# Optimization experiments

Hardware: AMD Instinct MI355X
Metric: run time of the kernel (lower is better)

Reference implementation:

```python
import jax, jax.numpy as jnp
import numpy as np
import math

B, H, S, D = 2, 16, 2048, 128
COEFF = 2.0  # layer_number


def setup_inputs() -> dict:
    key = jax.random.key(0)
    kq, kk, kv = jax.random.split(key, 3)
    return {
        "query_layer": jax.random.normal(kq, (B, H, S, D), dtype=jnp.float32),
        "key_layer": jax.random.normal(kk, (B, H, S, D), dtype=jnp.float32),
        "value_layer": jax.random.normal(kv, (B, H, S, D), dtype=jnp.float32),
    }


def reference(query_layer, key_layer, value_layer):
    b, h, sq, d = query_layer.shape
    sk = key_layer.shape[2]
    norm_factor = math.sqrt(d) * COEFF
    # raw scores [b,h,sq,sk]; divide by sqrt(d)*coeff, cast fp32, multiply by coeff
    scores = jnp.einsum("bhqd,bhkd->bhqk", query_layer, key_layer) / norm_factor
    scores = scores.astype(jnp.float32) * COEFF
    # causal mask (sq == sk path with attention_mask=None)
    causal = jnp.tril(jnp.ones((sq, sk), dtype=bool))
    scores = jnp.where(causal, scores, jnp.float32(-jnp.inf))
    probs = jax.nn.softmax(scores, axis=-1).astype(value_layer.dtype)
    # dropout p=0.0 -> identity
    ctx = jnp.einsum("bhqk,bhkd->bhqd", probs, value_layer)
    # [b,h,sq,d] -> [b,sq,h*d]
    return ctx.transpose(0, 2, 1, 3).reshape(b, sq, h * d)
```

## Files before the change

### kernel.cpp

```cpp
#include <hip/hip_runtime.h>
#include <hip/hip_bf16.h>
#include <math.h>

#define NB 2
#define NH 16
#define NS 2048
#define ND 128

typedef __bf16 bf16x8 __attribute__((ext_vector_type(8)));
typedef __bf16 bf16x4 __attribute__((ext_vector_type(4)));
typedef float f32x4 __attribute__((ext_vector_type(4)));

__global__ __launch_bounds__(256)
void prep(const float* __restrict__ K, const float* __restrict__ V,
          char* __restrict__ Kb, char* __restrict__ Vb)
{
    if (blockIdx.x < 4096) {
        int g = blockIdx.x * 256 + threadIdx.x;
        const int c8 = g & 15;
        const int row = g >> 4;
        const int s = row & 2047, bh = row >> 11;
        const int jt = s >> 6, r = s & 63;
        const float* src = K + ((size_t)row << 7) + (c8 << 3);
        float4 a = *(const float4*)src;
        float4 c = *(const float4*)(src + 4);
        bf16x8 o;
        o[0]=(__bf16)a.x; o[1]=(__bf16)a.y; o[2]=(__bf16)a.z; o[3]=(__bf16)a.w;
        o[4]=(__bf16)c.x; o[5]=(__bf16)c.y; o[6]=(__bf16)c.z; o[7]=(__bf16)c.w;
        *(bf16x8*)(Kb + (((size_t)(bh*32 + jt)) << 14) + r*256 + ((c8 ^ (r & 7)) << 4)) = o;
    } else {
        const int T    = blockIdx.x - 4096;
        const int w2   = threadIdx.x >> 6;
        const int lane = threadIdx.x & 63;
        const int d0   = lane << 1;
        const float2* vbase = (const float2*)V + ((size_t)T << 12);
        char* ob = Vb + ((size_t)T << 14);
        #pragma unroll
        for (int p = 0; p < 2; ++p) {
            const int kv8 = w2*2 + p;
            bf16x8 o0, o1;
            #pragma unroll
            for (int j = 0; j < 8; ++j) {
                float2 x = vbase[(size_t)(kv8*8 + j)*64 + lane];
                o0[j] = (__bf16)x.x;
                o1[j] = (__bf16)x.y;
            }
            *(bf16x8*)(ob + d0*128       + ((kv8 ^ (d0 & 7)) << 4))       = o0;
            *(bf16x8*)(ob + (d0+1)*128   + ((kv8 ^ ((d0+1) & 7)) << 4))   = o1;
        }
    }
}

__device__ __forceinline__ void gld16(void* lds, const void* gsrc)
{
    __builtin_amdgcn_global_load_lds(
        (const __attribute__((address_space(1))) void*)gsrc,
        (__attribute__((address_space(3))) void*)lds, 16, 0, 0);
}

__global__ __launch_bounds__(256, 2)
void fa_fwd(const float* __restrict__ Qg_, const char* __restrict__ Kb,
            const char* __restrict__ Vb, float* __restrict__ Out)
{
    __shared__ char Kl[2][16384];
    __shared__ char Vl[2][16384];
    __shared__ char Pl[8192];
    __shared__ float Rs[4][64];

    const int tid  = threadIdx.x;
    const int w    = tid >> 6;
    const int lane = tid & 63;
    const int quad = lane >> 4;
    const int l15  = lane & 15;

    const int pr = blockIdx.x >> 5;
    const int bh = blockIdx.x & 31;
    const int b  = bh >> 4, h = bh & 15;
    const int qtA = 31 - pr, qtB = pr;
    const int ntA = qtA + 1;
    const int total = ntA + qtB + 1;
    const int qA = qtA * 64, qB = qtB * 64;

    const float* Qg = Qg_ + (size_t)bh * NS * ND;
    const char*  Kt = Kb + ((size_t)bh << 19);
    const char*  Vt = Vb + ((size_t)bh << 19);

    const int xo = (l15 & 7) << 4;

    const float CSC = 0.08838834764831845f * 1.4426950408889634f;

    bf16x8 qf[4][4];
    auto loadQ = [&](int qbase) {
        #pragma unroll
        for (int nq = 0; nq < 4; ++nq) {
            const float* qp = Qg + (size_t)(qbase + nq*16 + l15) * ND + quad*8;
            #pragma unroll
            for (int ks = 0; ks < 4; ++ks) {
                float4 a = *(const float4*)(qp + ks*32);
                float4 c = *(const float4*)(qp + ks*32 + 4);
                bf16x8 f;
                f[0]=(__bf16)(a.x*CSC); f[1]=(__bf16)(a.y*CSC); f[2]=(__bf16)(a.z*CSC); f[3]=(__bf16)(a.w*CSC);
                f[4]=(__bf16)(c.x*CSC); f[5]=(__bf16)(c.y*CSC); f[6]=(__bf16)(c.z*CSC); f[7]=(__bf16)(c.w*CSC);
                qf[nq][ks] = f;
            }
        }
    };

    f32x4 O[4][2];
    float rs[4];
    #pragma unroll
    for (int m = 0; m < 4; ++m)
        #pragma unroll
        for (int nl = 0; nl < 2; ++nl)
            #pragma unroll
            for (int r = 0; r < 4; ++r) O[m][nl][r] = 0.0f;
    #pragma unroll
    for (int nq = 0; nq < 4; ++nq) rs[nq] = 0.0f;

    auto stage = [&](int jt, int buf) {
        const char* kg = Kt + (((size_t)jt) << 14) + w*4096 + lane*16;
        const char* vg = Vt + (((size_t)jt) << 14) + w*4096 + lane*16;
        char* kl = &Kl[buf][0] + w*4096;
        char* vl = &Vl[buf][0] + w*4096;
        #pragma unroll
        for (int i = 0; i < 4; ++i) {
            gld16(kl + i*1024, kg + i*1024);
            gld16(vl + i*1024, vg + i*1024);
        }
    };

    auto flush = [&](int qb) {
        #pragma unroll
        for (int nq = 0; nq < 4; ++nq) {
            float v = rs[nq];
            v += __shfl_xor(v, 16, 64);
            v += __shfl_xor(v, 32, 64);
            if (quad == 0) Rs[w][nq*16 + l15] = v;
        }
        __syncthreads();
        #pragma unroll
        for (int m = 0; m < 4; ++m) {
            #pragma unroll
            for (int r = 0; r < 4; ++r) {
                int qq = m*16 + quad*4 + r;
                float tt = Rs[0][qq] + Rs[1][qq] + Rs[2][qq] + Rs[3][qq];
                float inv = 1.0f / tt;
                int q = qb + qq;
                float* op = Out + ((size_t)(b*NS + q)) * (NH*ND) + h*ND + l15;
                op[(2*w)*16]   = O[m][0][r] * inv;
                op[(2*w+1)*16] = O[m][1][r] * inv;
            }
        }
    };

    loadQ(qA);
    stage(0, 0);
    int cur = 0;

    for (int t = 0; t < total; ++t) {
        const int phase = (t >= ntA);
        const bool diag = (phase ? (t - ntA) == qtB : t == qtA);

        if (t + 1 < total) {
            const int jt2 = (t + 1 >= ntA) ? (t + 1 - ntA) : (t + 1);
            stage(jt2, cur ^ 1);
            asm volatile("s_waitcnt vmcnt(8)" ::: "memory");
        } else {
            asm volatile("s_waitcnt vmcnt(0)" ::: "memory");
        }
        __builtin_amdgcn_s_barrier();
        asm volatile("" ::: "memory");

        if (t == ntA) {
            flush(qA);
            #pragma unroll
            for (int m = 0; m < 4; ++m)
                #pragma unroll
                for (int nl = 0; nl < 2; ++nl)
                    #pragma unroll
                    for (int r = 0; r < 4; ++r) O[m][nl][r] = 0.0f;
            #pragma unroll
            for (int nq = 0; nq < 4; ++nq) rs[nq] = 0.0f;
            loadQ(qB);
        }

        const char* Kc = &Kl[cur][0] + (w*16 + l15)*256;
        bf16x8 kf[4];
        #pragma unroll
        for (int ks = 0; ks < 4; ++ks)
            kf[ks] = *(const bf16x8*)(Kc + ((((ks*4 + quad) << 4)) ^ xo));
        f32x4 S[4];
        #pragma unroll
        for (int nq = 0; nq < 4; ++nq)
            #pragma unroll
            for (int r = 0; r < 4; ++r) S[nq][r] = 0.0f;
        __builtin_amdgcn_s_setprio(1);
        #pragma unroll
        for (int ks = 0; ks < 4; ++ks)
            #pragma unroll
            for (int nq = 0; nq < 4; ++nq)
                S[nq] = __builtin_amdgcn_mfma_f32_16x16x32_bf16(kf[ks], qf[nq][ks], S[nq], 0, 0, 0);
        __builtin_amdgcn_s_setprio(0);

        const char* Vc = &Vl[cur][0];
        bf16x8 vfr[2][2];
        #pragma unroll
        for (int nl = 0; nl < 2; ++nl)
            #pragma unroll
            for (int ks = 0; ks < 2; ++ks)
                vfr[nl][ks] = *(const bf16x8*)(Vc + ((2*w + nl)*16 + l15)*128 + ((((ks*4 + quad) << 4)) ^ xo));

        #pragma unroll
        for (int nq = 0; nq < 4; ++nq) {
            bf16x4 pk;
            #pragma unroll
            for (int r = 0; r < 4; ++r) {
                float e = exp2f(S[nq][r]);
                if (diag && (w*16 + quad*4 + r > nq*16 + l15)) e = 0.0f;
                rs[nq] += e;
                pk[r] = (__bf16)e;
            }
            *(bf16x4*)(Pl + (nq*16 + l15)*128 + ((((4*w + quad) ^ ((l15 & 7) << 1))) << 3)) = pk;
        }

        asm volatile("s_waitcnt lgkmcnt(0)" ::: "memory");
        __builtin_amdgcn_s_barrier();
        asm volatile("" ::: "memory");

        __builtin_amdgcn_s_setprio(1);
        #pragma unroll
        for (int m = 0; m < 4; ++m) {
            bf16x8 pa0 = *(const bf16x8*)(Pl + (m*16 + l15)*128 + (((quad << 4)) ^ xo));
            bf16x8 pa1 = *(const bf16x8*)(Pl + (m*16 + l15)*128 + ((((4 + quad) << 4)) ^ xo));
            O[m][0] = __builtin_amdgcn_mfma_f32_16x16x32_bf16(pa0, vfr[0][0], O[m][0], 0, 0, 0);
            O[m][1] = __builtin_amdgcn_mfma_f32_16x16x32_bf16(pa0, vfr[1][0], O[m][1], 0, 0, 0);
            O[m][0] = __builtin_amdgcn_mfma_f32_16x16x32_bf16(pa1, vfr[0][1], O[m][0], 0, 0, 0);
            O[m][1] = __builtin_amdgcn_mfma_f32_16x16x32_bf16(pa1, vfr[1][1], O[m][1], 0, 0, 0);
        }
        __builtin_amdgcn_s_setprio(0);

        asm volatile("" ::: "memory");
        __builtin_amdgcn_s_barrier();
        asm volatile("" ::: "memory");
        cur ^= 1;
    }

    flush(qB);
}

extern "C" void kernel_launch(void* const* d_in, const int* in_sizes, int n_in,
                              void* d_out, int out_size, void* d_ws, size_t ws_size,
                              hipStream_t stream) {
    const float* Q = (const float*)d_in[0];
    const float* K = (const float*)d_in[1];
    const float* V = (const float*)d_in[2];
    float* Out = (float*)d_out;
    char* Kb = (char*)d_ws;
    char* Vb = (char*)d_ws + ((size_t)32 << 19);
    prep<<<dim3(5120), dim3(256), 0, stream>>>(K, V, Kb, Vb);
    fa_fwd<<<dim3(512), dim3(256), 0, stream>>>(Q, Kb, Vb, Out);
}
```

Baseline: 202.0 us.

## Rewrite attention kernel with 32x32 MFMA, 128-row Q tiles and register-resident P

Measured after the change: 183.3 us. 1.1x faster.

```diff
diff --git a/kernel.cpp b/kernel.cpp
--- a/kernel.cpp
+++ b/kernel.cpp
@@ -8,8 +8,7 @@
 #define ND 128
 
 typedef __bf16 bf16x8 __attribute__((ext_vector_type(8)));
-typedef __bf16 bf16x4 __attribute__((ext_vector_type(4)));
-typedef float f32x4 __attribute__((ext_vector_type(4)));
+typedef float f32x16 __attribute__((ext_vector_type(16)));
 
 __global__ __launch_bounds__(256)
 void prep(const float* __restrict__ K, const float* __restrict__ V,
@@ -27,12 +26,11 @@
         bf16x8 o;
         o[0]=(__bf16)a.x; o[1]=(__bf16)a.y; o[2]=(__bf16)a.z; o[3]=(__bf16)a.w;
         o[4]=(__bf16)c.x; o[5]=(__bf16)c.y; o[6]=(__bf16)c.z; o[7]=(__bf16)c.w;
-        *(bf16x8*)(Kb + (((size_t)(bh*32 + jt)) << 14) + r*256 + ((c8 ^ (r & 7)) << 4)) = o;
+        *(bf16x8*)(Kb + (((size_t)(bh*32 + jt)) << 14) + r*256 + ((c8 ^ (r & 15)) << 4)) = o;
     } else {
         const int T    = blockIdx.x - 4096;
         const int w2   = threadIdx.x >> 6;
         const int lane = threadIdx.x & 63;
-        const int d0   = lane << 1;
         const float2* vbase = (const float2*)V + ((size_t)T << 12);
         char* ob = Vb + ((size_t)T << 14);
         #pragma unroll
@@ -45,8 +43,8 @@
                 o0[j] = (__bf16)x.x;
                 o1[j] = (__bf16)x.y;
             }
-            *(bf16x8*)(ob + d0*128       + ((kv8 ^ (d0 & 7)) << 4))       = o0;
-            *(bf16x8*)(ob + (d0+1)*128   + ((kv8 ^ ((d0+1) & 7)) << 4))   = o1;
+            *(bf16x8*)(ob + lane*256 + ((kv8 ^ (lane & 15)) << 4))       = o0;
+            *(bf16x8*)(ob + lane*256 + (((8 | kv8) ^ (lane & 15)) << 4)) = o1;
         }
     }
 }
@@ -62,190 +60,166 @@
 void fa_fwd(const float* __restrict__ Qg_, const char* __restrict__ Kb,
             const char* __restrict__ Vb, float* __restrict__ Out)
 {
-    __shared__ char Kl[2][16384];
-    __shared__ char Vl[2][16384];
-    __shared__ char Pl[8192];
-    __shared__ float Rs[4][64];
+    __shared__ char lds_[65536];
 
     const int tid  = threadIdx.x;
     const int w    = tid >> 6;
     const int lane = tid & 63;
-    const int quad = lane >> 4;
-    const int l15  = lane & 15;
-
-    const int pr = blockIdx.x >> 5;
-    const int bh = blockIdx.x & 31;
-    const int b  = bh >> 4, h = bh & 15;
-    const int qtA = 31 - pr, qtB = pr;
-    const int ntA = qtA + 1;
-    const int total = ntA + qtB + 1;
-    const int qA = qtA * 64, qB = qtB * 64;
+    const int l31  = lane & 31;
+    const int h    = lane >> 5;
+
+    const int c  = blockIdx.x;
+    const int bh = c & 31;
+    const int qt = (c < 256) ? (c >> 5) : (23 - (c >> 5));
+    const int b  = bh >> 4, head = bh & 15;
+    const int nt = 2 * (qt + 1);
+    const int qb = qt * 128;
+    const int qw = qb + 32 * w;
 
     const float* Qg = Qg_ + (size_t)bh * NS * ND;
     const char*  Kt = Kb + ((size_t)bh << 19);
     const char*  Vt = Vb + ((size_t)bh << 19);
 
-    const int xo = (l15 & 7) << 4;
+    int kaddr[8], vaddr[4];
+    #pragma unroll
+    for (int ks = 0; ks < 8; ++ks)
+        kaddr[ks] = l31*256 + (((2*ks + h) ^ (lane & 15)) << 4);
+    #pragma unroll
+    for (int ks = 0; ks < 4; ++ks)
+        vaddr[ks] = (l31 >> 1)*256 + (((((lane & 1) << 3) | (2*ks + h)) ^ (l31 >> 1)) << 4);
+
+    auto stage = [&](int t, int buf) {
+        const char* kg = Kt + (((size_t)t) << 14) + tid*16;
+        const char* vg = Vt + (((size_t)t) << 14) + tid*16;
+        char* kl = lds_ + buf*16384 + w*1024;
+        char* vl = lds_ + 32768 + buf*16384 + w*1024;
+        #pragma unroll
+        for (int i = 0; i < 4; ++i) gld16(kl + i*4096, kg + i*4096);
+        #pragma unroll
+        for (int i = 0; i < 4; ++i) gld16(vl + i*4096, vg + i*4096);
+    };
+
+    stage(0, 0);
+    stage(1, 1);
 
     const float CSC = 0.08838834764831845f * 1.4426950408889634f;
-
-    bf16x8 qf[4][4];
-    auto loadQ = [&](int qbase) {
-        #pragma unroll
-        for (int nq = 0; nq < 4; ++nq) {
-            const float* qp = Qg + (size_t)(qbase + nq*16 + l15) * ND + quad*8;
+    bf16x8 qf[8];
+    {
+        const float* qrow = Qg + (size_t)(qb + 32*w + l31) * ND + 8*h;
+        #pragma unroll
+        for (int ks = 0; ks < 8; ++ks) {
+            float4 a = *(const float4*)(qrow + 16*ks);
+            float4 d = *(const float4*)(qrow + 16*ks + 4);
+            bf16x8 f;
+            f[0]=(__bf16)(a.x*CSC); f[1]=(__bf16)(a.y*CSC); f[2]=(__bf16)(a.z*CSC); f[3]=(__bf16)(a.w*CSC);
+            f[4]=(__bf16)(d.x*CSC); f[5]=(__bf16)(d.y*CSC); f[6]=(__bf16)(d.z*CSC); f[7]=(__bf16)(d.w*CSC);
+            qf[ks] = f;
+        }
+    }
+
+    f32x16 O_[4];
+    #pragma unroll
+    for (int db = 0; db < 4; ++db)
+        #pragma unroll
+        for (int r = 0; r < 16; ++r) O_[db][r] = 0.0f;
+    float rs = 0.0f;
+
+    auto compute = [&](int t, int KIMM, int VIMM) {
+        f32x16 S0, S1;
+        #pragma unroll
+        for (int r = 0; r < 16; ++r) { S0[r] = 0.0f; S1[r] = 0.0f; }
+        __builtin_amdgcn_s_setprio(1);
+        #pragma unroll
+        for (int ks = 0; ks < 8; ++ks) {
+            bf16x8 ka = *(const bf16x8*)(lds_ + (kaddr[ks] + KIMM));
+            bf16x8 kb = *(const bf16x8*)(lds_ + (kaddr[ks] + KIMM + 8192));
+            S0 = __builtin_amdgcn_mfma_f32_32x32x16_bf16(ka, qf[ks], S0, 0, 0, 0);
+            S1 = __builtin_amdgcn_mfma_f32_32x32x16_bf16(kb, qf[ks], S1, 0, 0, 0);
+        }
+        __builtin_amdgcn_s_setprio(0);
+
+        if (64*t + 63 > qw) {
+            const int limh = qw + l31 - 64*t - 4*h;
             #pragma unroll
-            for (int ks = 0; ks < 4; ++ks) {
-                float4 a = *(const float4*)(qp + ks*32);
-                float4 c = *(const float4*)(qp + ks*32 + 4);
-                bf16x8 f;
-                f[0]=(__bf16)(a.x*CSC); f[1]=(__bf16)(a.y*CSC); f[2]=(__bf16)(a.z*CSC); f[3]=(__bf16)(a.w*CSC);
-                f[4]=(__bf16)(c.x*CSC); f[5]=(__bf16)(c.y*CSC); f[6]=(__bf16)(c.z*CSC); f[7]=(__bf16)(c.w*CSC);
-                qf[nq][ks] = f;
+            for (int r = 0; r < 16; ++r) {
+                const int k0 = (r & 3) + 8*(r >> 2);
+                if (k0 > limh)      S0[r] = -INFINITY;
+                if (k0 + 32 > limh) S1[r] = -INFINITY;
             }
         }
-    };
-
-    f32x4 O[4][2];
-    float rs[4];
-    #pragma unroll
-    for (int m = 0; m < 4; ++m)
-        #pragma unroll
-        for (int nl = 0; nl < 2; ++nl)
-            #pragma unroll
-            for (int r = 0; r < 4; ++r) O[m][nl][r] = 0.0f;
-    #pragma unroll
-    for (int nq = 0; nq < 4; ++nq) rs[nq] = 0.0f;
-
-    auto stage = [&](int jt, int buf) {
-        const char* kg = Kt + (((size_t)jt) << 14) + w*4096 + lane*16;
-        const char* vg = Vt + (((size_t)jt) << 14) + w*4096 + lane*16;
-        char* kl = &Kl[buf][0] + w*4096;
-        char* vl = &Vl[buf][0] + w*4096;
-        #pragma unroll
-        for (int i = 0; i < 4; ++i) {
-            gld16(kl + i*1024, kg + i*1024);
-            gld16(vl + i*1024, vg + i*1024);
-        }
-    };
-
-    auto flush = [&](int qb) {
-        #pragma unroll
-        for (int nq = 0; nq < 4; ++nq) {
-            float v = rs[nq];
-            v += __shfl_xor(v, 16, 64);
-            v += __shfl_xor(v, 32, 64);
-            if (quad == 0) Rs[w][nq*16 + l15] = v;
-        }
-        __syncthreads();
-        #pragma unroll
-        for (int m = 0; m < 4; ++m) {
-            #pragma unroll
-            for (int r = 0; r < 4; ++r) {
-                int qq = m*16 + quad*4 + r;
-                float tt = Rs[0][qq] + Rs[1][qq] + Rs[2][qq] + Rs[3][qq];
-                float inv = 1.0f / tt;
-                int q = qb + qq;
-                float* op = Out + ((size_t)(b*NS + q)) * (NH*ND) + h*ND + l15;
-                op[(2*w)*16]   = O[m][0][r] * inv;
-                op[(2*w+1)*16] = O[m][1][r] * inv;
-            }
-        }
-    };
-
-    loadQ(qA);
-    stage(0, 0);
-    int cur = 0;
-
-    for (int t = 0; t < total; ++t) {
-        const int phase = (t >= ntA);
-        const bool diag = (phase ? (t - ntA) == qtB : t == qtA);
-
-        if (t + 1 < total) {
-            const int jt2 = (t + 1 >= ntA) ? (t + 1 - ntA) : (t + 1);
-            stage(jt2, cur ^ 1);
-            asm volatile("s_waitcnt vmcnt(8)" ::: "memory");
-        } else {
-            asm volatile("s_waitcnt vmcnt(0)" ::: "memory");
-        }
-        __builtin_amdgcn_s_barrier();
-        asm volatile("" ::: "memory");
-
-        if (t == ntA) {
-            flush(qA);
-            #pragma unroll
-            for (int m = 0; m < 4; ++m)
-                #pragma unroll
-                for (int nl = 0; nl < 2; ++nl)
-                    #pragma unroll
-                    for (int r = 0; r < 4; ++r) O[m][nl][r] = 0.0f;
-            #pragma unroll
-            for (int nq = 0; nq < 4; ++nq) rs[nq] = 0.0f;
-            loadQ(qB);
-        }
-
-        const char* Kc = &Kl[cur][0] + (w*16 + l15)*256;
-        bf16x8 kf[4];
-        #pragma unroll
-        for (int ks = 0; ks < 4; ++ks)
-            kf[ks] = *(const bf16x8*)(Kc + ((((ks*4 + quad) << 4)) ^ xo));
-        f32x4 S[4];
-        #pragma unroll
-        for (int nq = 0; nq < 4; ++nq)
-            #pragma unroll
-            for (int r = 0; r < 4; ++r) S[nq][r] = 0.0f;
+        #pragma unroll
+        for (int r = 0; r < 16; ++r) {
+            float e0 = __builtin_amdgcn_exp2f(S0[r]);
+            float e1 = __builtin_amdgcn_exp2f(S1[r]);
+            rs += e0; rs += e1;
+            S0[r] = e0; S1[r] = e1;
+        }
+        unsigned P0[8], P1[8];
+        #pragma unroll
+        for (int i = 0; i < 8; ++i) {
+            unsigned u0, u1;
+            asm("v_cvt_pk_bf16_f32 %0, %1, %2" : "=v"(u0) : "v"(S0[2*i]), "v"(S0[2*i+1]));
+            asm("v_cvt_pk_bf16_f32 %0, %1, %2" : "=v"(u1) : "v"(S1[2*i]), "v"(S1[2*i+1]));
+            P0[i] = u0; P1[i] = u1;
+        }
+        bf16x8 pa[4];
+        #pragma unroll
+        for (int ks = 0; ks < 4; ++ks) {
+            const int o = 4*(ks & 1);
+            unsigned a0, a1, b0, b1;
+            if (ks < 2) { a0 = P0[o]; a1 = P0[o+1]; b0 = P0[o+2]; b1 = P0[o+3]; }
+            else        { a0 = P1[o]; a1 = P1[o+1]; b0 = P1[o+2]; b1 = P1[o+3]; }
+            asm("v_permlane32_swap_b32 %0, %1" : "+v"(a0), "+v"(b0));
+            asm("v_permlane32_swap_b32 %0, %1" : "+v"(a1), "+v"(b1));
+            union { unsigned u[4]; bf16x8 v; } cv;
+            cv.u[0] = a0; cv.u[1] = a1; cv.u[2] = b0; cv.u[3] = b1;
+            pa[ks] = cv.v;
+        }
         __builtin_amdgcn_s_setprio(1);
         #pragma unroll
         for (int ks = 0; ks < 4; ++ks)
             #pragma unroll
-            for (int nq = 0; nq < 4; ++nq)
-                S[nq] = __builtin_amdgcn_mfma_f32_16x16x32_bf16(kf[ks], qf[nq][ks], S[nq], 0, 0, 0);
+            for (int db = 0; db < 4; ++db) {
+                bf16x8 vf = *(const bf16x8*)(lds_ + (vaddr[ks] + VIMM + db*4096));
+                O_[db] = __builtin_amdgcn_mfma_f32_32x32x16_bf16(pa[ks], vf, O_[db], 0, 0, 0);
+            }
         __builtin_amdgcn_s_setprio(0);
-
-        const char* Vc = &Vl[cur][0];
-        bf16x8 vfr[2][2];
-        #pragma unroll
-        for (int nl = 0; nl < 2; ++nl)
-            #pragma unroll
-            for (int ks = 0; ks < 2; ++ks)
-                vfr[nl][ks] = *(const bf16x8*)(Vc + ((2*w + nl)*16 + l15)*128 + ((((ks*4 + quad) << 4)) ^ xo));
-
-        #pragma unroll
-        for (int nq = 0; nq < 4; ++nq) {
-            bf16x4 pk;
-            #pragma unroll
-            for (int r = 0; r < 4; ++r) {
-                float e = exp2f(S[nq][r]);
-                if (diag && (w*16 + quad*4 + r > nq*16 + l15)) e = 0.0f;
-                rs[nq] += e;
-                pk[r] = (__bf16)e;
-            }
-            *(bf16x4*)(Pl + (nq*16 + l15)*128 + ((((4*w + quad) ^ ((l15 & 7) << 1))) << 3)) = pk;
-        }
-
-        asm volatile("s_waitcnt lgkmcnt(0)" ::: "memory");
-        __builtin_amdgcn_s_barrier();
-        asm volatile("" ::: "memory");
-
-        __builtin_amdgcn_s_setprio(1);
-        #pragma unroll
-        for (int m = 0; m < 4; ++m) {
-            bf16x8 pa0 = *(const bf16x8*)(Pl + (m*16 + l15)*128 + (((quad << 4)) ^ xo));
-            bf16x8 pa1 = *(const bf16x8*)(Pl + (m*16 + l15)*128 + ((((4 + quad) << 4)) ^ xo));
-            O[m][0] = __builtin_amdgcn_mfma_f32_16x16x32_bf16(pa0, vfr[0][0], O[m][0], 0, 0, 0);
-            O[m][1] = __builtin_amdgcn_mfma_f32_16x16x32_bf16(pa0, vfr[1][0], O[m][1], 0, 0, 0);
-            O[m][0] = __builtin_amdgcn_mfma_f32_16x16x32_bf16(pa1, vfr[0][1], O[m][0], 0, 0, 0);
-            O[m][1] = __builtin_amdgcn_mfma_f32_16x16x32_bf16(pa1, vfr[1][1], O[m][1], 0, 0, 0);
-        }
-        __builtin_amdgcn_s_setprio(0);
-
-        asm volatile("" ::: "memory");
-        __builtin_amdgcn_s_barrier();
-        asm volatile("" ::: "memory");
-        cur ^= 1;
+    };
+
+    for (int t = 0; t < nt; t += 2) {
+        asm volatile("s_waitcnt vmcnt(8)" ::: "memory");
+        __builtin_amdgcn_s_barrier();
+        asm volatile("" ::: "memory");
+        if (64*t <= qw + 31) compute(t, 0, 32768);
+        asm volatile("" ::: "memory");
+        __builtin_amdgcn_s_barrier();
+        asm volatile("" ::: "memory");
+        if (t + 2 < nt) stage(t + 2, 0);
+        if (t + 2 < nt) { asm volatile("s_waitcnt vmcnt(8)" ::: "memory"); }
+        else            { asm volatile("s_waitcnt vmcnt(0)" ::: "memory"); }
+        __builtin_amdgcn_s_barrier();
+        asm volatile("" ::: "memory");
+        if (64*(t+1) <= qw + 31) compute(t + 1, 16384, 49152);
+        asm volatile("" ::: "memory");
+        __builtin_amdgcn_s_barrier();
+        asm volatile("" ::: "memory");
+        if (t + 3 < nt) stage(t + 3, 1);
     }
 
-    flush(qB);
+    float tot = rs + __shfl_xor(rs, 32, 64);
+    float inv = 1.0f / tot;
+    float fi[16];
+    #pragma unroll
+    for (int r = 0; r < 16; ++r)
+        fi[r] = __shfl(inv, (r & 3) + 8*(r >> 2) + 4*h, 64);
+    float* op = Out + ((size_t)(b*NS + qb + 32*w)) * (NH*ND) + head*ND + l31;
+    #pragma unroll
+    for (int db = 0; db < 4; ++db)
+        #pragma unroll
+        for (int r = 0; r < 16; ++r) {
+            const int qloc = (r & 3) + 8*(r >> 2) + 4*h;
+            op[(size_t)qloc * (NH*ND) + db*32] = O_[db][r] * fi[r];
+        }
 }
 
 extern "C" void kernel_launch(void* const* d_in, const int* in_sizes, int n_in,
```
